# Optimization experiments

Hardware: AMD Instinct MI355X
Metric: run time of the kernel (lower is better)

Reference implementation:

```python
import jax, jax.numpy as jnp
import numpy as np

V, E, H = 1024, 32, 64
D = 8                     # number of tree levels (root at depth 0)
PER = 149796              # nodes per non-root level
N = 1 + 7 * PER           # 1048573 total nodes


def setup_inputs() -> dict:
    rng = np.random.default_rng(0)
    sizes = [1] + [PER] * (D - 1)
    off = np.concatenate([[0], np.cumsum(sizes)])
    depth = np.repeat(np.arange(D), sizes).astype(np.int64)
    parent = np.zeros(N, dtype=np.int64)  # root points to itself (harmless: its h is 0 when read)
    for l in range(1, D):
        parent[off[l]:off[l + 1]] = rng.integers(off[l - 1], off[l], sizes[l])
    token_ids = rng.integers(0, V, N).astype(np.int64)

    key = jax.random.key(0)
    ks = jax.random.split(key, 7)
    s = 0.05
    return {
        "token_ids": jnp.asarray(token_ids),
        "parent": jnp.asarray(parent),
        "depth": jnp.asarray(depth),
        "max_depth": D - 1,
        "emb": jax.random.normal(ks[0], (V, E), jnp.float32) * s,
        "W_iou_w": jax.random.normal(ks[1], (3 * H, E), jnp.float32) * s,
        "W_iou_b": jax.random.normal(ks[2], (3 * H,), jnp.float32) * s,
        "U_iou_w": jax.random.normal(ks[3], (3 * H, H), jnp.float32) * s,
        "W_f_w": jax.random.normal(ks[4], (H, E), jnp.float32) * s,
        "W_f_b": jax.random.normal(ks[5], (H,), jnp.float32) * s,
        "U_f_w": jax.random.normal(ks[6], (H, H), jnp.float32) * s,
    }


def reference(token_ids, parent, depth, max_depth, emb,
              W_iou_w, W_iou_b, U_iou_w, W_f_w, W_f_b, U_f_w):
    n = token_ids.shape[0]
    hid = U_f_w.shape[0]
    x = emb[token_ids]                                 # [N, E]
    wiou_x = x @ W_iou_w.T + W_iou_b                   # [N, 3H] (input part, precomputed)
    wf_x = x @ W_f_w.T + W_f_b                         # [N, H]
    h = jnp.zeros((n, hid), x.dtype)
    c = jnp.zeros((n, hid), x.dtype)
    # level-synchronous bottom-up sweep (deepest level first); children of a
    # depth-d node are exactly at depth d+1, already finalized when d is processed
    for d in range(max_depth, -1, -1):
        h_sum = jax.ops.segment_sum(h, parent, num_segments=n)        # child-sum per parent
        f = jax.nn.sigmoid(wf_x[parent] + h @ U_f_w.T)                # forget gate per child edge
        fc = jax.ops.segment_sum(f * c, parent, num_segments=n)      # sum_k f_k * c_k per parent
        iou = wiou_x + h_sum @ U_iou_w.T
        i, o, u = jnp.split(iou, 3, axis=-1)
        c_new = jax.nn.sigmoid(i) * jnp.tanh(u) + fc
        h_new = jax.nn.sigmoid(o) * jnp.tanh(c_new)
        m = (depth == d)[:, None]
        h = jnp.where(m, h_new, h)
        c = jnp.where(m, c_new, c)
    return h[0]  # root hidden state, matching TreeLSTMEncoder.forward
```

## Files before the change

### kernel.cpp

```cpp
#include <hip/hip_runtime.h>

#define PER  149796
#define NN   1048573
#define HDIM 64
#define EDIM 32
#define NIOU 192
#define STG  96

typedef _Float16 f16;
typedef _Float16 f16x8 __attribute__((ext_vector_type(8)));
typedef _Float16 f16x4 __attribute__((ext_vector_type(4)));
typedef _Float16 f16x2 __attribute__((ext_vector_type(2)));
typedef float    f32x4 __attribute__((ext_vector_type(4)));

typedef __attribute__((address_space(1))) const unsigned gu32;
typedef __attribute__((address_space(3))) unsigned lu32;

__device__ __forceinline__ float sigf(float x){ return 1.0f/(1.0f+__expf(-x)); }
__device__ __forceinline__ float tanh_f(float x){
  float ax = fabsf(x);
  float e  = __expf(-2.0f*ax);
  float t  = (1.0f - e)/(1.0f + e);
  return x < 0.0f ? -t : t;
}

__global__ __launch_bounds__(256) void countAll_kernel(const int* __restrict__ parent,
                                                       int* __restrict__ cnt){
  int idx = blockIdx.x*256 + threadIdx.x;
  if (idx >= 6*PER) return;
  atomicAdd(&cnt[parent[1 + PER + idx]], 1);
}

__device__ __forceinline__ int cnt_at(const int* cnt, int idx){
  return (idx == 0) ? PER : cnt[idx];
}

__global__ __launch_bounds__(256) void scan1_kernel(const int* __restrict__ cnt, int* __restrict__ bsum){
  __shared__ int sc[256];
  int b = blockIdx.x, t = threadIdx.x;
  int base = b*1024 + t*4;
  int s = 0;
  #pragma unroll
  for (int e=0;e<4;e++){ int idx=base+e; if (idx<NN) s += cnt_at(cnt, idx); }
  sc[t]=s; __syncthreads();
  for (int d=128; d>0; d>>=1){ if (t<d) sc[t]+=sc[t+d]; __syncthreads(); }
  if (t==0) bsum[b]=sc[0];
}

__global__ __launch_bounds__(1024) void scan2_kernel(const int* __restrict__ bsum, int* __restrict__ bbase){
  __shared__ int sc[1024];
  int t=threadIdx.x;
  sc[t]=bsum[t]; __syncthreads();
  for (int d=1; d<1024; d<<=1){
    int v = (t>=d)? sc[t-d] : 0; __syncthreads();
    sc[t]+=v; __syncthreads();
  }
  bbase[t] = (t==0)?0:sc[t-1];
}

__global__ __launch_bounds__(256) void scan3_kernel(const int* __restrict__ cnt, const int* __restrict__ bbase,
                                                    int* __restrict__ off, int* __restrict__ cursor){
  __shared__ int sc[256];
  int b=blockIdx.x, t=threadIdx.x;
  int base=b*1024+t*4;
  int e0 = (base  <NN)?cnt_at(cnt,base  ):0;
  int e1 = (base+1<NN)?cnt_at(cnt,base+1):0;
  int e2 = (base+2<NN)?cnt_at(cnt,base+2):0;
  int e3 = (base+3<NN)?cnt_at(cnt,base+3):0;
  int tsum=e0+e1+e2+e3;
  sc[t]=tsum; __syncthreads();
  for (int d=1; d<256; d<<=1){
    int v=(t>=d)?sc[t-d]:0; __syncthreads();
    sc[t]+=v; __syncthreads();
  }
  int x = bbase[b] + ((t==0)?0:sc[t-1]);
  if (base  <NN){ off[base  ]=x;          cursor[base  ]=x; }
  if (base+1<NN){ off[base+1]=x+e0;       cursor[base+1]=x+e0; }
  if (base+2<NN){ off[base+2]=x+e0+e1;    cursor[base+2]=x+e0+e1; }
  if (base+3<NN){ off[base+3]=x+e0+e1+e2; cursor[base+3]=x+e0+e1+e2; }
}

__global__ __launch_bounds__(256) void scatterAll_kernel(const int* __restrict__ parent,
    const int* __restrict__ tok, int* __restrict__ cursor,
    int* __restrict__ childpos, int* __restrict__ ptok){
  int idx = blockIdx.x*256 + threadIdx.x;
  if (idx >= 6*PER) return;
  int g = 1 + PER + idx;
  int jp = parent[g];
  int pos = atomicAdd(&cursor[jp], 1);
  childpos[g] = pos;
  ptok[pos] = tok[jp];
}

__global__ __launch_bounds__(256) void tablepack_kernel(
    const float* __restrict__ emb, const float* __restrict__ Wiou, const float* __restrict__ biou,
    const float* __restrict__ Wf, const float* __restrict__ bf,
    const float* __restrict__ Uf, const float* __restrict__ Uiou,
    float* __restrict__ embWiou, float* __restrict__ embWf,
    f16* __restrict__ Bfp, f16* __restrict__ Biop)
{
  if (blockIdx.x < 1024){
    int v = blockIdx.x;
    int m = threadIdx.x;
    const float* x = emb + (size_t)v*EDIM;
    if (m < NIOU){
      float a = biou[m];
      #pragma unroll
      for (int e=0;e<EDIM;e++) a += Wiou[m*EDIM+e]*x[e];
      embWiou[(size_t)v*NIOU + m] = a;
    } else {
      int mm = m - NIOU;
      float a = bf[mm];
      #pragma unroll
      for (int e=0;e<EDIM;e++) a += Wf[mm*EDIM+e]*x[e];
      embWf[(size_t)v*HDIM + mm] = a;
    }
  } else {
    for (int i = threadIdx.x; i < 2*4*64*8; i += 256){
      int j = i & 7, L = (i>>3)&63, st = i>>9;
      int t = st & 3, s = st >> 2;
      int k = s*32 + (L>>4)*8 + j;
      int n = t*16 + (L&15);
      Bfp[i] = (f16)Uf[n*HDIM + k];
    }
    for (int i = threadIdx.x; i < 2*12*64*8; i += 256){
      int j = i & 7, L = (i>>3)&63, st = i>>9;
      int t = st % 12, s = st / 12;
      int k = s*32 + (L>>4)*8 + j;
      int n = t*16 + (L&15);
      Biop[i] = (f16)Uiou[n*HDIM + k];
    }
  }
}

__global__ __launch_bounds__(256) void leafA_kernel(
    const int* __restrict__ tok, const int* __restrict__ childpos,
    const float* __restrict__ embWiou, f16* __restrict__ Htmp,
    f16x2* __restrict__ HF, float* __restrict__ Ctmp)
{
  int gid = blockIdx.x*256 + threadIdx.x;
  if (gid >= PER*16) return;
  int j = gid >> 4, sub = gid & 15;
  int g = 1 + 6*PER + j;
  int t = tok[g];
  const float* row = embWiou + (size_t)t*NIOU;
  float4 i4 = *(const float4*)(row + sub*4);
  float4 o4 = *(const float4*)(row + 64 + sub*4);
  float4 u4 = *(const float4*)(row + 128 + sub*4);
  float4 cv; f16x4 hv;
  cv.x = sigf(i4.x)*tanh_f(u4.x); hv.x = (f16)(sigf(o4.x)*tanh_f(cv.x));
  cv.y = sigf(i4.y)*tanh_f(u4.y); hv.y = (f16)(sigf(o4.y)*tanh_f(cv.y));
  cv.z = sigf(i4.z)*tanh_f(u4.z); hv.z = (f16)(sigf(o4.z)*tanh_f(cv.z));
  cv.w = sigf(i4.w)*tanh_f(u4.w); hv.w = (f16)(sigf(o4.w)*tanh_f(cv.w));
  int pos = childpos[g] - 6*PER;
  *(float4*)(Ctmp + (size_t)pos*HDIM + sub*4) = cv;
  *(f16x4*)(Htmp + (size_t)pos*HDIM + sub*4) = hv;
  f16x2* hf = HF + (size_t)pos*HDIM + sub*4;
  hf[0].x = hv.x; hf[1].x = hv.y; hf[2].x = hv.z; hf[3].x = hv.w;
}

__global__ __launch_bounds__(256) void leafB_kernel(
    const int* __restrict__ ptok, const float* __restrict__ embWf, const f16* __restrict__ Ufpack,
    const f16* __restrict__ Htmp, const float* __restrict__ Ctmp, f16x2* __restrict__ HF)
{
  int lane = threadIdx.x & 63;
  int wv   = threadIdx.x >> 6;
  int base = (blockIdx.x*4 + wv)*64;
  if (base >= PER) return;
  int q = lane >> 4, c16 = lane & 15;
  const f16x8* Bp = (const f16x8*)Ufpack;
  f16x8 B[2][4];
  #pragma unroll
  for (int s=0;s<2;s++)
    #pragma unroll
    for (int t=0;t<4;t++) B[s][t] = Bp[(s*4+t)*64 + lane];
  f32x4 acc[4][4];
  #pragma unroll
  for (int a=0;a<4;a++)
    #pragma unroll
    for (int b=0;b<4;b++) acc[a][b] = (f32x4){0.f,0.f,0.f,0.f};
  #pragma unroll
  for (int tm=0;tm<4;tm++){
    int r0 = base + tm*16 + c16;
    if (r0 > PER-1) r0 = PER-1;
    const f16* hp = Htmp + (size_t)r0*HDIM;
    f16x8 A0 = *(const f16x8*)(hp + q*8);
    f16x8 A1 = *(const f16x8*)(hp + 32 + q*8);
    #pragma unroll
    for (int nt=0;nt<4;nt++){
      acc[tm][nt] = __builtin_amdgcn_mfma_f32_16x16x32_f16(A0, B[0][nt], acc[tm][nt], 0,0,0);
      acc[tm][nt] = __builtin_amdgcn_mfma_f32_16x16x32_f16(A1, B[1][nt], acc[tm][nt], 0,0,0);
    }
  }
  #pragma unroll
  for (int tm=0;tm<4;tm++){
    #pragma unroll
    for (int r=0;r<4;r++){
      int lrow = base + tm*16 + q*4 + r;
      bool ok = lrow < PER;
      int rl = ok ? lrow : PER-1;
      int wt = ptok[6*PER + rl];
      const float* wr = embWf + (size_t)wt*HDIM;
      #pragma unroll
      for (int nt=0;nt<4;nt++){
        int col = nt*16 + c16;
        float gg = acc[tm][nt][r] + wr[col];
        float v = sigf(gg) * Ctmp[(size_t)rl*HDIM + col];
        if (ok) HF[(size_t)rl*HDIM + col].y = (f16)v;
      }
    }
  }
}

__global__ __launch_bounds__(256) void node_fused(
    const int* __restrict__ tok, const int* __restrict__ off,
    const int* __restrict__ childpos, const int* __restrict__ ptok,
    const float* __restrict__ embWiou, const float* __restrict__ embWf,
    const f16* __restrict__ Biopack, const f16* __restrict__ Ufpack,
    const f16x2* __restrict__ HFin, f16x2* __restrict__ HFout,
    int poff, int relbase, int outbase, int identityOut)
{
  __shared__ f16x2 stage[STG*64];
  __shared__ f16   Ah[64*72];
  __shared__ float FAs[64*68];
  int lane = threadIdx.x & 63;
  int wv   = __builtin_amdgcn_readfirstlane(threadIdx.x >> 6);
  int p0   = wv*16;
  int j0b  = blockIdx.x*64;
  int j0   = j0b + p0;
  int ei = j0b + 64; if (ei > PER) ei = PER;
  int S = off[poff + j0b] - relbase;
  int E = off[poff + ei]  - relbase;
  int sB[17];
  #pragma unroll
  for (int i=0;i<=16;i++){
    int jj = j0 + i; if (jj > PER) jj = PER;
    sB[i] = off[poff + jj] - relbase;
  }
  float hs[16], fa[16];
  #pragma unroll
  for (int i=0;i<16;i++){ hs[i]=0.f; fa[i]=0.f; }
  const unsigned* HFinU = (const unsigned*)HFin;
  for (int cb = S; cb < E; cb += STG){
    int n = E - cb; if (n > STG) n = STG;
    for (int r = wv; r < n; r += 4){
      gu32* gp = (gu32*)(HFinU + (size_t)(cb+r)*HDIM) + lane;
      __builtin_amdgcn_global_load_lds(gp, (lu32*)&stage[r*HDIM], 4, 0, 0);
    }
    __syncthreads();
    int lim = cb + n;
    #pragma unroll
    for (int i=0;i<16;i++){
      int lo = sB[i]   > cb  ? sB[i]   : cb;
      int hi = sB[i+1] < lim ? sB[i+1] : lim;
      for (int p=lo; p<hi; ++p){
        f16x2 v = stage[(p-cb)*HDIM + lane];
        hs[i] += (float)v.x; fa[i] += (float)v.y;
      }
    }
    __syncthreads();
  }
  #pragma unroll
  for (int i=0;i<16;i++){
    Ah[(p0+i)*72 + lane]  = (f16)hs[i];
    FAs[(p0+i)*68 + lane] = fa[i];
  }
  __syncthreads();
  int q = lane>>4, c16 = lane&15;
  f16x8 A0 = *(const f16x8*)(Ah + (p0+c16)*72 + q*8);
  f16x8 A1 = *(const f16x8*)(Ah + (p0+c16)*72 + 32 + q*8);
  const f16x8* Bp = (const f16x8*)Biopack;
  f32x4 acc[12];
  #pragma unroll
  for (int nt=0;nt<12;nt++) acc[nt] = (f32x4){0.f,0.f,0.f,0.f};
  #pragma unroll
  for (int nt=0;nt<12;nt++){
    f16x8 B0 = Bp[nt*64 + lane];
    f16x8 B1 = Bp[(12+nt)*64 + lane];
    acc[nt] = __builtin_amdgcn_mfma_f32_16x16x32_f16(A0, B0, acc[nt], 0,0,0);
    acc[nt] = __builtin_amdgcn_mfma_f32_16x16x32_f16(A1, B1, acc[nt], 0,0,0);
  }
  int tok0 = identityOut ? tok[0] : 0;
  float cc[4][4];
  f16   hh[4][4];
  int   opos_[4]; int wt_[4]; bool ok_[4];
  #pragma unroll
  for (int r=0;r<4;r++){
    int j = j0 + q*4 + r;
    bool ok = j < PER;
    int jl = ok ? j : PER-1;
    int g = poff + jl;
    int tk = tok[g];
    const float* tr = embWiou + (size_t)tk*NIOU;
    int opg = identityOut ? (outbase + jl) : childpos[g];
    int op  = opg - outbase;
    opos_[r]=op; ok_[r]=ok;
    wt_[r] = identityOut ? tok0 : ptok[opg];
    int prow = p0 + q*4 + r;
    #pragma unroll
    for (int nt=0;nt<4;nt++){
      int col = nt*16 + c16;
      float ai = acc[nt][r]   + tr[col];
      float ao = acc[nt+4][r] + tr[64+col];
      float au = acc[nt+8][r] + tr[128+col];
      float fav = FAs[prow*68 + col];
      float c = sigf(ai)*tanh_f(au) + fav;
      float h = sigf(ao)*tanh_f(c);
      cc[r][nt] = c;
      hh[r][nt] = (f16)h;
    }
  }
  __syncthreads();
  #pragma unroll
  for (int r=0;r<4;r++)
    #pragma unroll
    for (int nt=0;nt<4;nt++)
      Ah[(p0+q*4+r)*72 + nt*16 + c16] = hh[r][nt];
  __syncthreads();
  f16x8 H0 = *(const f16x8*)(Ah + (p0+c16)*72 + q*8);
  f16x8 H1 = *(const f16x8*)(Ah + (p0+c16)*72 + 32 + q*8);
  const f16x8* Up = (const f16x8*)Ufpack;
  f32x4 g4[4];
  #pragma unroll
  for (int nt=0;nt<4;nt++) g4[nt] = (f32x4){0.f,0.f,0.f,0.f};
  #pragma unroll
  for (int nt=0;nt<4;nt++){
    f16x8 B0 = Up[nt*64 + lane];
    f16x8 B1 = Up[(4+nt)*64 + lane];
    g4[nt] = __builtin_amdgcn_mfma_f32_16x16x32_f16(H0, B0, g4[nt], 0,0,0);
    g4[nt] = __builtin_amdgcn_mfma_f32_16x16x32_f16(H1, B1, g4[nt], 0,0,0);
  }
  #pragma unroll
  for (int r=0;r<4;r++){
    if (!ok_[r]) continue;
    const float* wr = embWf + (size_t)wt_[r]*HDIM;
    int op = opos_[r];
    #pragma unroll
    for (int nt=0;nt<4;nt++){
      int col = nt*16 + c16;
      float v = sigf(g4[nt][r] + wr[col]) * cc[r][nt];
      f16x2 o; o.x = hh[r][nt]; o.y = (f16)v;
      HFout[(size_t)op*HDIM + col] = o;
    }
  }
}

__global__ __launch_bounds__(256) void rootred_kernel(
    const f16x2* __restrict__ HFin, float* __restrict__ rootacc)
{
  int t = blockIdx.x*blockDim.x + threadIdx.x;
  int m = t & 63;
  int j0 = t >> 6;
  int jstep = (gridDim.x*blockDim.x) >> 6;
  float af=0.f, ah=0.f;
  for (int j=j0; j<PER; j+=jstep){
    f16x2 v = HFin[(size_t)j*HDIM + m];
    ah += (float)v.x;
    af += (float)v.y;
  }
  __shared__ float red[256];
  red[threadIdx.x]=af; __syncthreads();
  if (threadIdx.x < 64) atomicAdd(&rootacc[m],    red[m]+red[64+m]+red[128+m]+red[192+m]);
  __syncthreads();
  red[threadIdx.x]=ah; __syncthreads();
  if (threadIdx.x < 64) atomicAdd(&rootacc[64+m], red[m]+red[64+m]+red[128+m]+red[192+m]);
}

__global__ void rootnode_kernel(
    const int* __restrict__ tok, const float* __restrict__ emb,
    const float* __restrict__ Wiou, const float* __restrict__ biou, const float* __restrict__ Uiou,
    const float* __restrict__ rootacc, float* __restrict__ out)
{
  int m = threadIdx.x;
  if (m >= HDIM) return;
  int t = tok[0];
  float ai=biou[m], ao=biou[HDIM+m], au=biou[2*HDIM+m];
  for (int e=0;e<EDIM;e++){
    float xe = emb[(size_t)t*EDIM+e];
    ai += Wiou[(size_t)m*EDIM+e]*xe;
    ao += Wiou[(size_t)(HDIM+m)*EDIM+e]*xe;
    au += Wiou[(size_t)(2*HDIM+m)*EDIM+e]*xe;
  }
  for (int k=0;k<HDIM;k++){
    float hv = rootacc[64+k];
    ai += Uiou[(size_t)m*HDIM+k]*hv;
    ao += Uiou[(size_t)(HDIM+m)*HDIM+k]*hv;
    au += Uiou[(size_t)(2*HDIM+m)*HDIM+k]*hv;
  }
  float c = sigf(ai)*tanh_f(au) + rootacc[m];
  out[m] = sigf(ao)*tanh_f(c);
}

static inline char* alignup(char* p){
  uintptr_t u = (uintptr_t)p;
  u = (u + 255) & ~(uintptr_t)255;
  return (char*)u;
}

extern "C" void kernel_launch(void* const* d_in, const int* in_sizes, int n_in,
                              void* d_out, int out_size, void* d_ws, size_t ws_size,
                              hipStream_t stream)
{
  const int*   tok    = (const int*)d_in[0];
  const int*   parent = (const int*)d_in[1];
  const float* emb    = (const float*)d_in[4];
  const float* Wiou   = (const float*)d_in[5];
  const float* biou   = (const float*)d_in[6];
  const float* Uiou   = (const float*)d_in[7];
  const float* Wf     = (const float*)d_in[8];
  const float* bf     = (const float*)d_in[9];
  const float* Uf     = (const float*)d_in[10];
  float* out = (float*)d_out;

  char* w = (char*)d_ws;
  f16x2* HFA     = (f16x2*)w;  w = alignup(w + (size_t)PER*HDIM*sizeof(f16x2));
  f16x2* HFB     = (f16x2*)w;  w = alignup(w + (size_t)PER*HDIM*sizeof(f16x2));
  f16*   Htmp    = (f16*)w;    w = alignup(w + (size_t)PER*HDIM*sizeof(f16));
  float* Ctmp    = (float*)w;  w = alignup(w + (size_t)PER*HDIM*sizeof(float));
  int*   cnt     = (int*)w;    w = alignup(w + (size_t)NN*sizeof(int));
  int*   off     = (int*)w;    w = alignup(w + (size_t)NN*sizeof(int));
  int*   cursor  = (int*)w;    w = alignup(w + (size_t)NN*sizeof(int));
  int*   childpos= (int*)w;    w = alignup(w + (size_t)NN*sizeof(int));
  int*   ptok    = (int*)w;    w = alignup(w + (size_t)NN*sizeof(int));
  int*   bsum    = (int*)w;    w = alignup(w + 1024*sizeof(int));
  int*   bbase   = (int*)w;    w = alignup(w + 1024*sizeof(int));
  float* embWiou = (float*)w;  w = alignup(w + 1024*NIOU*sizeof(float));
  float* embWf   = (float*)w;  w = alignup(w + 1024*HDIM*sizeof(float));
  float* rootacc = (float*)w;  w = alignup(w + 128*sizeof(float));
  f16*   Ufpack  = (f16*)w;    w = alignup(w + 2*4*64*8*sizeof(f16));
  f16*   Biopack = (f16*)w;    w = alignup(w + 2*12*64*8*sizeof(f16));

  const int gPER = (PER + 255)/256;
  const int gALL = (6*PER + 255)/256;

  hipMemsetAsync(cnt, 0, (size_t)(1 + 6*PER)*sizeof(int), stream);
  hipMemsetAsync(rootacc, 0, 128*sizeof(float), stream);

  countAll_kernel  <<<gALL, 256, 0, stream>>>(parent, cnt);
  scan1_kernel     <<<1024, 256, 0, stream>>>(cnt, bsum);
  scan2_kernel     <<<1, 1024, 0, stream>>>(bsum, bbase);
  scan3_kernel     <<<1024, 256, 0, stream>>>(cnt, bbase, off, cursor);
  scatterAll_kernel<<<gALL, 256, 0, stream>>>(parent, tok, cursor, childpos, ptok);
  tablepack_kernel <<<1025, 256, 0, stream>>>(emb, Wiou, biou, Wf, bf, Uf, Uiou,
                                              embWiou, embWf, Ufpack, Biopack);

  leafA_kernel<<<(PER*16 + 255)/256, 256, 0, stream>>>(tok, childpos, embWiou, Htmp, HFA, Ctmp);
  leafB_kernel<<<gPER, 256, 0, stream>>>(ptok, embWf, Ufpack, Htmp, Ctmp, HFA);

  f16x2* HFin = HFA; f16x2* HFou = HFB;
  for (int d=6; d>=1; --d){
    int poff = 1 + (d-1)*PER;
    node_fused<<<(PER + 63)/64, 256, 0, stream>>>(tok, off, childpos, ptok,
                                                  embWiou, embWf, Biopack, Ufpack,
                                                  HFin, HFou,
                                                  poff, d*PER, (d-1)*PER, (d==1) ? 1 : 0);
    f16x2* th=HFin; HFin=HFou; HFou=th;
  }

  rootred_kernel<<<256, 256, 0, stream>>>(HFin, rootacc);
  rootnode_kernel<<<1, 64, 0, stream>>>(tok, emb, Wiou, biou, Uiou, rootacc, out);
}
```

Baseline: 592.5 us.

## Handle leaf level inside node_fused and alias LDS buffers with f16 forget sums

The separate leafA and leafB kernels are removed. The leaf level (depth 7) now runs through node_fused with a leafLevel flag that skips the child gather, so its child sums are zero. This drops the Htmp and Ctmp intermediates and one launch. Shared memory is also unioned: the Ah and forget-accumulator arrays alias the staging buffer, and the forget sums are stored as f16 instead of f32, which reduces LDS use per block and could raise occupancy. The cost is the extra f16 rounding on fc, plus running the heavier fused kernel for leaves in place of the lighter leafA element-wise pass.

```diff
diff --git a/kernel.cpp b/kernel.cpp
--- a/kernel.cpp
+++ b/kernel.cpp
@@ -133,137 +133,63 @@
   }
 }
 
-__global__ __launch_bounds__(256) void leafA_kernel(
-    const int* __restrict__ tok, const int* __restrict__ childpos,
-    const float* __restrict__ embWiou, f16* __restrict__ Htmp,
-    f16x2* __restrict__ HF, float* __restrict__ Ctmp)
-{
-  int gid = blockIdx.x*256 + threadIdx.x;
-  if (gid >= PER*16) return;
-  int j = gid >> 4, sub = gid & 15;
-  int g = 1 + 6*PER + j;
-  int t = tok[g];
-  const float* row = embWiou + (size_t)t*NIOU;
-  float4 i4 = *(const float4*)(row + sub*4);
-  float4 o4 = *(const float4*)(row + 64 + sub*4);
-  float4 u4 = *(const float4*)(row + 128 + sub*4);
-  float4 cv; f16x4 hv;
-  cv.x = sigf(i4.x)*tanh_f(u4.x); hv.x = (f16)(sigf(o4.x)*tanh_f(cv.x));
-  cv.y = sigf(i4.y)*tanh_f(u4.y); hv.y = (f16)(sigf(o4.y)*tanh_f(cv.y));
-  cv.z = sigf(i4.z)*tanh_f(u4.z); hv.z = (f16)(sigf(o4.z)*tanh_f(cv.z));
-  cv.w = sigf(i4.w)*tanh_f(u4.w); hv.w = (f16)(sigf(o4.w)*tanh_f(cv.w));
-  int pos = childpos[g] - 6*PER;
-  *(float4*)(Ctmp + (size_t)pos*HDIM + sub*4) = cv;
-  *(f16x4*)(Htmp + (size_t)pos*HDIM + sub*4) = hv;
-  f16x2* hf = HF + (size_t)pos*HDIM + sub*4;
-  hf[0].x = hv.x; hf[1].x = hv.y; hf[2].x = hv.z; hf[3].x = hv.w;
-}
-
-__global__ __launch_bounds__(256) void leafB_kernel(
-    const int* __restrict__ ptok, const float* __restrict__ embWf, const f16* __restrict__ Ufpack,
-    const f16* __restrict__ Htmp, const float* __restrict__ Ctmp, f16x2* __restrict__ HF)
-{
-  int lane = threadIdx.x & 63;
-  int wv   = threadIdx.x >> 6;
-  int base = (blockIdx.x*4 + wv)*64;
-  if (base >= PER) return;
-  int q = lane >> 4, c16 = lane & 15;
-  const f16x8* Bp = (const f16x8*)Ufpack;
-  f16x8 B[2][4];
-  #pragma unroll
-  for (int s=0;s<2;s++)
-    #pragma unroll
-    for (int t=0;t<4;t++) B[s][t] = Bp[(s*4+t)*64 + lane];
-  f32x4 acc[4][4];
-  #pragma unroll
-  for (int a=0;a<4;a++)
-    #pragma unroll
-    for (int b=0;b<4;b++) acc[a][b] = (f32x4){0.f,0.f,0.f,0.f};
-  #pragma unroll
-  for (int tm=0;tm<4;tm++){
-    int r0 = base + tm*16 + c16;
-    if (r0 > PER-1) r0 = PER-1;
-    const f16* hp = Htmp + (size_t)r0*HDIM;
-    f16x8 A0 = *(const f16x8*)(hp + q*8);
-    f16x8 A1 = *(const f16x8*)(hp + 32 + q*8);
-    #pragma unroll
-    for (int nt=0;nt<4;nt++){
-      acc[tm][nt] = __builtin_amdgcn_mfma_f32_16x16x32_f16(A0, B[0][nt], acc[tm][nt], 0,0,0);
-      acc[tm][nt] = __builtin_amdgcn_mfma_f32_16x16x32_f16(A1, B[1][nt], acc[tm][nt], 0,0,0);
-    }
-  }
-  #pragma unroll
-  for (int tm=0;tm<4;tm++){
-    #pragma unroll
-    for (int r=0;r<4;r++){
-      int lrow = base + tm*16 + q*4 + r;
-      bool ok = lrow < PER;
-      int rl = ok ? lrow : PER-1;
-      int wt = ptok[6*PER + rl];
-      const float* wr = embWf + (size_t)wt*HDIM;
-      #pragma unroll
-      for (int nt=0;nt<4;nt++){
-        int col = nt*16 + c16;
-        float gg = acc[tm][nt][r] + wr[col];
-        float v = sigf(gg) * Ctmp[(size_t)rl*HDIM + col];
-        if (ok) HF[(size_t)rl*HDIM + col].y = (f16)v;
-      }
-    }
-  }
-}
-
 __global__ __launch_bounds__(256) void node_fused(
     const int* __restrict__ tok, const int* __restrict__ off,
     const int* __restrict__ childpos, const int* __restrict__ ptok,
     const float* __restrict__ embWiou, const float* __restrict__ embWf,
     const f16* __restrict__ Biopack, const f16* __restrict__ Ufpack,
     const f16x2* __restrict__ HFin, f16x2* __restrict__ HFout,
-    int poff, int relbase, int outbase, int identityOut)
-{
-  __shared__ f16x2 stage[STG*64];
-  __shared__ f16   Ah[64*72];
-  __shared__ float FAs[64*68];
+    int poff, int relbase, int outbase, int identityOut, int leafLevel)
+{
+  __shared__ __align__(16) char smem[STG*HDIM*4];
+  f16x2* stage = (f16x2*)smem;
+  f16*   Ah    = (f16*)smem;
+  f16*   FAf   = (f16*)(smem + 9216);
   int lane = threadIdx.x & 63;
   int wv   = __builtin_amdgcn_readfirstlane(threadIdx.x >> 6);
   int p0   = wv*16;
   int j0b  = blockIdx.x*64;
   int j0   = j0b + p0;
-  int ei = j0b + 64; if (ei > PER) ei = PER;
-  int S = off[poff + j0b] - relbase;
-  int E = off[poff + ei]  - relbase;
-  int sB[17];
-  #pragma unroll
-  for (int i=0;i<=16;i++){
-    int jj = j0 + i; if (jj > PER) jj = PER;
-    sB[i] = off[poff + jj] - relbase;
-  }
+
   float hs[16], fa[16];
   #pragma unroll
   for (int i=0;i<16;i++){ hs[i]=0.f; fa[i]=0.f; }
-  const unsigned* HFinU = (const unsigned*)HFin;
-  for (int cb = S; cb < E; cb += STG){
-    int n = E - cb; if (n > STG) n = STG;
-    for (int r = wv; r < n; r += 4){
-      gu32* gp = (gu32*)(HFinU + (size_t)(cb+r)*HDIM) + lane;
-      __builtin_amdgcn_global_load_lds(gp, (lu32*)&stage[r*HDIM], 4, 0, 0);
-    }
-    __syncthreads();
-    int lim = cb + n;
+
+  if (!leafLevel){
+    int ei = j0b + 64; if (ei > PER) ei = PER;
+    int S = off[poff + j0b] - relbase;
+    int E = off[poff + ei]  - relbase;
+    int sB[17];
     #pragma unroll
-    for (int i=0;i<16;i++){
-      int lo = sB[i]   > cb  ? sB[i]   : cb;
-      int hi = sB[i+1] < lim ? sB[i+1] : lim;
-      for (int p=lo; p<hi; ++p){
-        f16x2 v = stage[(p-cb)*HDIM + lane];
-        hs[i] += (float)v.x; fa[i] += (float)v.y;
+    for (int i=0;i<=16;i++){
+      int jj = j0 + i; if (jj > PER) jj = PER;
+      sB[i] = off[poff + jj] - relbase;
+    }
+    const unsigned* HFinU = (const unsigned*)HFin;
+    for (int cb = S; cb < E; cb += STG){
+      int n = E - cb; if (n > STG) n = STG;
+      for (int r = wv; r < n; r += 4){
+        gu32* gp = (gu32*)(HFinU + (size_t)(cb+r)*HDIM) + lane;
+        __builtin_amdgcn_global_load_lds(gp, (lu32*)&stage[r*HDIM], 4, 0, 0);
       }
-    }
-    __syncthreads();
+      __syncthreads();
+      int lim = cb + n;
+      #pragma unroll
+      for (int i=0;i<16;i++){
+        int lo = sB[i]   > cb  ? sB[i]   : cb;
+        int hi = sB[i+1] < lim ? sB[i+1] : lim;
+        for (int p=lo; p<hi; ++p){
+          f16x2 v = stage[(p-cb)*HDIM + lane];
+          hs[i] += (float)v.x; fa[i] += (float)v.y;
+        }
+      }
+      __syncthreads();
+    }
   }
   #pragma unroll
   for (int i=0;i<16;i++){
     Ah[(p0+i)*72 + lane]  = (f16)hs[i];
-    FAs[(p0+i)*68 + lane] = fa[i];
+    FAf[(p0+i)*68 + lane] = (f16)fa[i];
   }
   __syncthreads();
   int q = lane>>4, c16 = lane&15;
@@ -303,7 +229,7 @@
       float ai = acc[nt][r]   + tr[col];
       float ao = acc[nt+4][r] + tr[64+col];
       float au = acc[nt+8][r] + tr[128+col];
-      float fav = FAs[prow*68 + col];
+      float fav = (float)FAf[prow*68 + col];
       float c = sigf(ai)*tanh_f(au) + fav;
       float h = sigf(ao)*tanh_f(c);
       cc[r][nt] = c;
@@ -415,8 +341,6 @@
   char* w = (char*)d_ws;
   f16x2* HFA     = (f16x2*)w;  w = alignup(w + (size_t)PER*HDIM*sizeof(f16x2));
   f16x2* HFB     = (f16x2*)w;  w = alignup(w + (size_t)PER*HDIM*sizeof(f16x2));
-  f16*   Htmp    = (f16*)w;    w = alignup(w + (size_t)PER*HDIM*sizeof(f16));
-  float* Ctmp    = (float*)w;  w = alignup(w + (size_t)PER*HDIM*sizeof(float));
   int*   cnt     = (int*)w;    w = alignup(w + (size_t)NN*sizeof(int));
   int*   off     = (int*)w;    w = alignup(w + (size_t)NN*sizeof(int));
   int*   cursor  = (int*)w;    w = alignup(w + (size_t)NN*sizeof(int));
@@ -430,7 +354,6 @@
   f16*   Ufpack  = (f16*)w;    w = alignup(w + 2*4*64*8*sizeof(f16));
   f16*   Biopack = (f16*)w;    w = alignup(w + 2*12*64*8*sizeof(f16));
 
-  const int gPER = (PER + 255)/256;
   const int gALL = (6*PER + 255)/256;
 
   hipMemsetAsync(cnt, 0, (size_t)(1 + 6*PER)*sizeof(int), stream);
@@ -444,19 +367,22 @@
   tablepack_kernel <<<1025, 256, 0, stream>>>(emb, Wiou, biou, Wf, bf, Uf, Uiou,
                                               embWiou, embWf, Ufpack, Biopack);
 
-  leafA_kernel<<<(PER*16 + 255)/256, 256, 0, stream>>>(tok, childpos, embWiou, Htmp, HFA, Ctmp);
-  leafB_kernel<<<gPER, 256, 0, stream>>>(ptok, embWf, Ufpack, Htmp, Ctmp, HFA);
-
-  f16x2* HFin = HFA; f16x2* HFou = HFB;
-  for (int d=6; d>=1; --d){
+  f16x2* bufs[2] = {HFA, HFB};
+  int outIdx = 0;
+  f16x2* last = HFA;
+  for (int d=7; d>=1; --d){
     int poff = 1 + (d-1)*PER;
+    f16x2* in  = bufs[1-outIdx];
+    f16x2* ou  = bufs[outIdx];
     node_fused<<<(PER + 63)/64, 256, 0, stream>>>(tok, off, childpos, ptok,
                                                   embWiou, embWf, Biopack, Ufpack,
-                                                  HFin, HFou,
-                                                  poff, d*PER, (d-1)*PER, (d==1) ? 1 : 0);
-    f16x2* th=HFin; HFin=HFou; HFou=th;
-  }
-
-  rootred_kernel<<<256, 256, 0, stream>>>(HFin, rootacc);
+                                                  in, ou,
+                                                  poff, d*PER, (d-1)*PER,
+                                                  (d==1) ? 1 : 0, (d==7) ? 1 : 0);
+    last = ou;
+    outIdx ^= 1;
+  }
+
+  rootred_kernel<<<256, 256, 0, stream>>>(last, rootacc);
   rootnode_kernel<<<1, 64, 0, stream>>>(tok, emb, Wiou, biou, Uiou, rootacc, out);
 }
```

New measurement: 594.7 us. No clear change (+0.4%).
